# Performance work log

Measured on AMD Instinct MI355X. Metric: run time of the kernel, lower is better.

## Reference

```python
import jax, jax.numpy as jnp
import numpy as np

N, E, F_IN, HID, HEADS, G = 50000, 800000, 128, 128, 4, 512
NEG_SLOPE = 0.2


def setup_inputs() -> dict:
    key = jax.random.key(0)
    ks = jax.random.split(key, 16)
    x = jax.random.normal(ks[0], (N, F_IN), dtype=jnp.float32)
    edge_index = jax.random.randint(ks[1], (2, E), 0, N, dtype=jnp.int32)
    batch = jnp.sort(jax.random.randint(ks[2], (N,), 0, G, dtype=jnp.int32))
    s1 = 1.0 / np.sqrt(F_IN)
    s2 = 1.0 / np.sqrt(HEADS * HID)
    params = {
        "W1": jax.random.uniform(ks[3], (F_IN, HEADS * HID), jnp.float32, -s1, s1),
        "a_src1": jax.random.normal(ks[4], (HEADS, HID), jnp.float32) * s1,
        "a_dst1": jax.random.normal(ks[5], (HEADS, HID), jnp.float32) * s1,
        "b1": jnp.zeros((HEADS * HID,), jnp.float32),
        "W2": jax.random.uniform(ks[6], (HEADS * HID, HID), jnp.float32, -s2, s2),
        "a_src2": jax.random.normal(ks[7], (1, HID), jnp.float32) * s2,
        "a_dst2": jax.random.normal(ks[8], (1, HID), jnp.float32) * s2,
        "b2": jnp.zeros((HID,), jnp.float32),
        "Wl": jax.random.normal(ks[9], (HID, 1), jnp.float32) / np.sqrt(HID),
        "bl": jnp.zeros((1,), jnp.float32),
    }
    return dict(x=x, edge_index=edge_index, batch=batch, **params)


def _gat_conv(x, W, a_src, a_dst, b, src, dst, heads, out_ch):
    n = x.shape[0]
    h = (x @ W).reshape(n, heads, out_ch)                      # [N,H,C]
    asrc = jnp.sum(h * a_src, axis=-1)                          # [N,H]
    adst = jnp.sum(h * a_dst, axis=-1)                          # [N,H]
    logits = jax.nn.leaky_relu(asrc[src] + adst[dst], NEG_SLOPE)  # [E,H]
    m = jax.ops.segment_max(logits, dst, num_segments=n)        # stable softmax per dst
    e = jnp.exp(logits - m[dst])
    denom = jax.ops.segment_sum(e, dst, num_segments=n)
    alpha = e / denom[dst]                                      # [E,H]
    out = jax.ops.segment_sum(alpha[:, :, None] * h[src], dst, num_segments=n)
    return out.reshape(n, heads * out_ch) + b


def reference(x, edge_index, batch, W1, a_src1, a_dst1, b1, W2, a_src2, a_dst2, b2, Wl, bl):
    n = x.shape[0]
    loop = jnp.arange(n, dtype=edge_index.dtype)
    src = jnp.concatenate([edge_index[0], loop])  # add_self_loops=True (PyG default)
    dst = jnp.concatenate([edge_index[1], loop])
    h = _gat_conv(x, W1, a_src1, a_dst1, b1, src, dst, HEADS, HID)
    h = jax.nn.elu(h)
    h = _gat_conv(h, W2, a_src2, a_dst2, b2, src, dst, 1, HID)
    h = jax.nn.elu(h)
    # global_mean_pool
    sums = jax.ops.segment_sum(h, batch, num_segments=G)
    cnts = jax.ops.segment_sum(jnp.ones((n,), h.dtype), batch, num_segments=G)
    pooled = sums / jnp.maximum(cnts, 1.0)[:, None]
    return (pooled @ Wl + bl).squeeze()
```

## Files before the change

### kernel.cpp

```cpp
#include <hip/hip_runtime.h>
#include <math.h>

#define NEG_SLOPE 0.2f

typedef float f4 __attribute__((ext_vector_type(4)));
typedef __attribute__((ext_vector_type(8))) short short8;
typedef __attribute__((ext_vector_type(4))) float f32x4;
typedef unsigned short ushort_t;
typedef unsigned char uchar_t;

__device__ __forceinline__ float bf2f(unsigned short s) {
    unsigned u = ((unsigned)s) << 16;
    float f; __builtin_memcpy(&f, &u, 4); return f;
}
__device__ __forceinline__ unsigned short f2bf(float f) {
    unsigned u; __builtin_memcpy(&u, &f, 4);
    u = (u + 0x7FFFu + ((u >> 16) & 1u)) >> 16;
    return (unsigned short)u;
}
__device__ __forceinline__ void gload16(const void* g, void* l) {
    __builtin_amdgcn_global_load_lds((const __attribute__((address_space(1))) void*)g,
                                     (__attribute__((address_space(3))) void*)l, 16, 0, 0);
}
__device__ __forceinline__ void cvt4(unsigned u, float& a, float& b, float& c, float& d) {
    asm("v_cvt_f32_ubyte0 %0, %1" : "=v"(a) : "v"(u));
    asm("v_cvt_f32_ubyte1 %0, %1" : "=v"(b) : "v"(u));
    asm("v_cvt_f32_ubyte2 %0, %1" : "=v"(c) : "v"(u));
    asm("v_cvt_f32_ubyte3 %0, %1" : "=v"(d) : "v"(u));
}

__global__ void hist_kernel(const int* __restrict__ ei, int E, int Et, int* __restrict__ deg) {
    int e = blockIdx.x * blockDim.x + threadIdx.x;
    if (e >= Et) return;
    int d = (e < E) ? ei[E + e] : (e - E);
    atomicAdd(&deg[d], 1);
}

__global__ __launch_bounds__(1024) void scan_local(const int* __restrict__ deg,
                                                   int* __restrict__ off,
                                                   int* __restrict__ btot, int n) {
    __shared__ int s_w[16];
    int tid = threadIdx.x, lane = tid & 63, wv = tid >> 6;
    int i = blockIdx.x * 1024 + tid;
    int v = (i < n) ? deg[i] : 0;
    int x = v;
    #pragma unroll
    for (int d = 1; d < 64; d <<= 1) {
        int y = __shfl_up(x, d);
        if (lane >= d) x += y;
    }
    if (lane == 63) s_w[wv] = x;
    __syncthreads();
    if (tid < 16) {
        int y = s_w[tid];
        int z = y;
        #pragma unroll
        for (int d = 1; d < 16; d <<= 1) {
            int t2 = __shfl_up(z, d);
            if (tid >= d) z += t2;
        }
        if (tid == 15) btot[blockIdx.x] = z;
        s_w[tid] = z - y;
    }
    __syncthreads();
    if (i < n) off[i] = s_w[wv] + (x - v);
}

__global__ void scan_base(int* __restrict__ btot, int nb) {
    int lane = threadIdx.x;
    int v = (lane < nb) ? btot[lane] : 0;
    int x = v;
    #pragma unroll
    for (int d = 1; d < 64; d <<= 1) {
        int y = __shfl_up(x, d);
        if (lane >= d) x += y;
    }
    int total = __shfl(x, nb - 1);
    if (lane < nb) btot[lane] = x - v;
    if (lane == 0) btot[nb] = total;
}

__global__ void scan_add(const int* __restrict__ btot, int* __restrict__ off,
                         int* __restrict__ cur, const int* __restrict__ batch,
                         int* __restrict__ gcnt, int n, int nb) {
    int i = blockIdx.x * blockDim.x + threadIdx.x;
    if (i < n) {
        int o = off[i] + btot[i >> 10];
        off[i] = o;
        cur[i] = o;
        atomicAdd(&gcnt[batch[i]], 1);
    } else if (i == n) {
        off[n] = btot[nb];
    }
}

__global__ void scatter_kernel(const int* __restrict__ ei, int E, int Et,
                               int* __restrict__ cur, int* __restrict__ csr) {
    int e = blockIdx.x * blockDim.x + threadIdx.x;
    if (e >= Et) return;
    int s, d;
    if (e < E) { s = ei[e]; d = ei[E + e]; }
    else       { s = d = e - E; }
    int p = atomicAdd(&cur[d], 1);
    csr[p] = s;
}

__global__ void cast_all(const float* __restrict__ x, const float* __restrict__ W1,
                         const float* __restrict__ W2, ushort_t* __restrict__ xb,
                         ushort_t* __restrict__ W1t, ushort_t* __restrict__ W2t,
                         int n_x, int pad_x) {
    int i = blockIdx.x * blockDim.x + threadIdx.x;
    if (i < pad_x) {
        xb[i] = f2bf(i < n_x ? x[i] : 0.f);
        return;
    }
    int k = i - pad_x;
    if (k < 128 * 512) {
        int r = k >> 9, c = k & 511;
        W1t[(size_t)c * 128 + r] = f2bf(W1[k]);
        return;
    }
    k -= 128 * 512;
    if (k < 512 * 128) {
        int r = k >> 7, c = k & 127;
        W2t[(size_t)c * 512 + r] = f2bf(W2[k]);
    }
}

template<int H>
__global__ __launch_bounds__(256) void gemm_q128(const ushort_t* __restrict__ A,
                                                 const ushort_t* __restrict__ Bt,
                                                 uchar_t* __restrict__ Cq,
                                                 const float* __restrict__ aw_src,
                                                 const float* __restrict__ aw_dst,
                                                 float* __restrict__ side,
                                                 float* __restrict__ avd,
                                                 int K) {
    const int Nc = H * 128;
    __shared__ __align__(16) ushort_t As[128 * 32];
    __shared__ __align__(16) ushort_t Bs[128 * 32];
    __shared__ float s_red[3][2][128];
    __shared__ float s_rs[128];
    __shared__ __align__(16) uchar_t s_q[128 * 144];
    const int t = threadIdx.x, w = t >> 6, lane = t & 63;
    const int r0 = blockIdx.x * 128, hb = blockIdx.y, c0 = hb * 128;
    const int wr = w & 1, wc = w >> 1;

    const ushort_t* Ag = A + (size_t)(r0 + w * 32 + (lane >> 2)) * K + (lane & 3) * 8;
    const ushort_t* Bg = Bt + (size_t)(c0 + w * 32 + (lane >> 2)) * K + (lane & 3) * 8;
    ushort_t* Al = As + w * 1024;
    ushort_t* Bl = Bs + w * 1024;

    f32x4 acc[4][4] = {};
    for (int k0 = 0; k0 < K; k0 += 32) {
        __syncthreads();
        gload16(Ag + k0, Al);
        gload16(Ag + k0 + (size_t)16 * K, Al + 512);
        gload16(Bg + k0, Bl);
        gload16(Bg + k0 + (size_t)16 * K, Bl + 512);
        __syncthreads();
        short8 af[4], bf[4];
        #pragma unroll
        for (int i = 0; i < 4; i++) {
            af[i] = *(const short8*)(As + (wr * 64 + i * 16 + (lane & 15)) * 32 + (lane >> 4) * 8);
            bf[i] = *(const short8*)(Bs + (wc * 64 + i * 16 + (lane & 15)) * 32 + (lane >> 4) * 8);
        }
        #pragma unroll
        for (int i = 0; i < 4; i++)
            #pragma unroll
            for (int jj = 0; jj < 4; jj++)
                acc[i][jj] = __builtin_amdgcn_mfma_f32_16x16x32_bf16(af[i], bf[jj], acc[i][jj], 0, 0, 0);
    }

    float asc[4], adc[4];
    #pragma unroll
    for (int jj = 0; jj < 4; jj++) {
        int c = c0 + wc * 64 + jj * 16 + (lane & 15);
        asc[jj] = aw_src[c];
        adc[jj] = aw_dst[c];
    }
    #pragma unroll
    for (int i = 0; i < 4; i++) {
        #pragma unroll
        for (int r = 0; r < 4; r++) {
            float m = 0.f, ps = 0.f, pd = 0.f;
            #pragma unroll
            for (int jj = 0; jj < 4; jj++) {
                float v = acc[i][jj][r];
                m = fmaxf(m, fabsf(v));
                ps = fmaf(v, asc[jj], ps);
                pd = fmaf(v, adc[jj], pd);
            }
            #pragma unroll
            for (int d = 1; d < 16; d <<= 1) {
                m = fmaxf(m, __shfl_xor(m, d));
                ps += __shfl_xor(ps, d);
                pd += __shfl_xor(pd, d);
            }
            if ((lane & 15) == 0) {
                int row = wr * 64 + i * 16 + (lane >> 4) * 4 + r;
                s_red[0][wc][row] = m;
                s_red[1][wc][row] = ps;
                s_red[2][wc][row] = pd;
            }
        }
    }
    __syncthreads();
    if (t < 128) {
        float rm = fmaxf(fmaxf(s_red[0][0][t], s_red[0][1][t]), 1e-30f);
        s_rs[t] = 127.f / rm;
        int node = r0 + t;
        side[(size_t)node * (2 * H) + hb]     = s_red[1][0][t] + s_red[1][1][t];
        side[(size_t)node * (2 * H) + H + hb] = rm * (1.f / 127.f);
        avd[(size_t)node * H + hb]            = s_red[2][0][t] + s_red[2][1][t];
    }
    __syncthreads();
    #pragma unroll
    for (int i = 0; i < 4; i++)
        #pragma unroll
        for (int jj = 0; jj < 4; jj++)
            #pragma unroll
            for (int r = 0; r < 4; r++) {
                int row = wr * 64 + i * 16 + (lane >> 4) * 4 + r;
                int col = wc * 64 + jj * 16 + (lane & 15);
                int qi = (int)rintf(acc[i][jj][r] * s_rs[row]) + 128;
                qi = min(255, max(0, qi));
                s_q[row * 144 + col] = (uchar_t)qi;
            }
    __syncthreads();
    #pragma unroll
    for (int p2 = 0; p2 < 4; p2++) {
        int idx = p2 * 256 + t;
        int row = idx >> 3, ch = idx & 7;
        *(uint4*)(Cq + (size_t)(r0 + row) * Nc + c0 + ch * 16) =
            *(const uint4*)(s_q + row * 144 + ch * 16);
    }
}

template<int H, int TOT, bool OUT_BF16>
__global__ __launch_bounds__(256) void agg_q(const int* __restrict__ off,
                                             const int* __restrict__ csr,
                                             const uchar_t* __restrict__ fq,
                                             const float* __restrict__ side,
                                             const float* __restrict__ avd,
                                             const float* __restrict__ bias,
                                             void* __restrict__ outv, int n) {
    constexpr int J = TOT / 64;
    __shared__ float s_e[4][64 * H];
    __shared__ float s_es[4][64 * H];
    int w = threadIdx.x >> 6, lane = threadIdx.x & 63;
    int dst = blockIdx.x * 4 + w;
    if (dst >= n) return;
    const int h_own = (H == 1) ? 0 : (lane >> 4);
    float adv[H];
    if constexpr (H == 4) {
        f4 t4 = *(const f4*)&avd[(size_t)dst * 4];
        #pragma unroll
        for (int h = 0; h < 4; h++) adv[h] = t4[h];
    } else {
        adv[0] = avd[dst];
    }
    int beg = off[dst], end = off[dst + 1];
    float den = 0.f, Ssum = 0.f;
    float acc[J] = {};
    float* ew  = s_e[w];
    float* esw = s_es[w];

    for (int b = beg; b < end; b += 64) {
        int idx = b + lane;
        bool val = idx < end;
        int sv = val ? csr[idx] : 0;
        unsigned myoff = (unsigned)sv * TOT;
        if constexpr (H == 4) {
            const f4* sp = (const f4*)(side + (size_t)sv * 8);
            f4 av = sp[0], sc = sp[1];
            f4 ev, esv;
            #pragma unroll
            for (int h = 0; h < 4; h++) {
                float l = av[h] + adv[h];
                l = fmaxf(l, l * NEG_SLOPE);
                float e = val ? __expf(l) : 0.f;
                ev[h] = e;
                esv[h] = e * sc[h];
            }
            *(f4*)&ew[lane * 4]  = ev;
            *(f4*)&esw[lane * 4] = esv;
        } else {
            float2 sp = *(const float2*)(side + (size_t)sv * 2);
            float l = sp.x + adv[0];
            l = fmaxf(l, l * NEG_SLOPE);
            float e = val ? __expf(l) : 0.f;
            ew[lane]  = e;
            esw[lane] = e * sp.y;
        }
        asm volatile("s_waitcnt lgkmcnt(0)" ::: "memory");
        int cnt = min(64, end - b);
        for (int jb = 0; jb < cnt; jb += 8) {
            uint2 u8v[8];
            unsigned us16[8];
            #pragma unroll
            for (int q = 0; q < 8; q++) {
                unsigned o = (unsigned)__builtin_amdgcn_readlane((int)myoff, jb + q);
                if constexpr (J == 8) {
                    u8v[q] = *(const uint2*)(fq + o + lane * 8);
                } else {
                    us16[q] = *(const ushort_t*)(fq + o + lane * 2);
                }
            }
            #pragma unroll
            for (int q = 0; q < 8; q++) {
                int j = jb + q;
                float e  = ew[j * H + h_own];
                float es = esw[j * H + h_own];
                den += e;
                Ssum += es;
                if constexpr (J == 8) {
                    float b0, b1, b2, b3;
                    cvt4(u8v[q].x, b0, b1, b2, b3);
                    acc[0] = fmaf(es, b0, acc[0]);
                    acc[1] = fmaf(es, b1, acc[1]);
                    acc[2] = fmaf(es, b2, acc[2]);
                    acc[3] = fmaf(es, b3, acc[3]);
                    cvt4(u8v[q].y, b0, b1, b2, b3);
                    acc[4] = fmaf(es, b0, acc[4]);
                    acc[5] = fmaf(es, b1, acc[5]);
                    acc[6] = fmaf(es, b2, acc[6]);
                    acc[7] = fmaf(es, b3, acc[7]);
                } else {
                    float b0, b1;
                    asm("v_cvt_f32_ubyte0 %0, %1" : "=v"(b0) : "v"(us16[q]));
                    asm("v_cvt_f32_ubyte1 %0, %1" : "=v"(b1) : "v"(us16[q]));
                    acc[0] = fmaf(es, b0, acc[0]);
                    acc[1] = fmaf(es, b1, acc[1]);
                }
            }
        }
    }
    float rden = 1.f / den;
    if constexpr (OUT_BF16) {
        unsigned short ov[J];
        #pragma unroll
        for (int u = 0; u < J; u++) {
            float v = (acc[u] - 128.f * Ssum) * rden + bias[lane * J + u];
            v = v > 0.f ? v : expm1f(v);
            ov[u] = f2bf(v);
        }
        *(short8*)((ushort_t*)outv + (size_t)dst * TOT + lane * J) = *(short8*)ov;
    } else {
        float v0 = (acc[0] - 128.f * Ssum) * rden + bias[lane * 2];
        float v1 = (acc[1] - 128.f * Ssum) * rden + bias[lane * 2 + 1];
        v0 = v0 > 0.f ? v0 : expm1f(v0);
        v1 = v1 > 0.f ? v1 : expm1f(v1);
        float2 vv = make_float2(v0, v1);
        *(float2*)((float*)outv + (size_t)dst * TOT + lane * 2) = vv;
    }
}

__global__ __launch_bounds__(256) void pool_kernel(const float* __restrict__ feat,
                                                   const int* __restrict__ batch,
                                                   float* __restrict__ gsum, int n) {
    int t = threadIdx.x;
    int ch = t & 127, half = t >> 7;
    int base = blockIdx.x * 64;
    float acc = 0.f;
    int curg = -1;
    for (int k = half; k < 64; k += 2) {
        int node = base + k;
        if (node >= n) break;
        int g = batch[node];
        if (g != curg) {
            if (curg >= 0) atomicAdd(&gsum[(size_t)curg * 128 + ch], acc);
            acc = 0.f;
            curg = g;
        }
        acc += feat[(size_t)node * 128 + ch];
    }
    if (curg >= 0) atomicAdd(&gsum[(size_t)curg * 128 + ch], acc);
}

__global__ __launch_bounds__(256) void final_kernel(const float* __restrict__ gsum,
                                                    const int* __restrict__ gcnt,
                                                    const float* __restrict__ Wl,
                                                    const float* __restrict__ bl,
                                                    float* __restrict__ out, int g_total) {
    int w = threadIdx.x >> 6, lane = threadIdx.x & 63;
    int g = blockIdx.x * 4 + w;
    if (g >= g_total) return;
    float inv = 1.f / fmaxf((float)gcnt[g], 1.f);
    float p = 0.f;
    #pragma unroll
    for (int j = 0; j < 2; j++) {
        int ch = lane + 64 * j;
        p += gsum[(size_t)g * 128 + ch] * Wl[ch];
    }
    #pragma unroll
    for (int d = 32; d; d >>= 1) p += __shfl_xor(p, d);
    if (lane == 0) out[g] = p * inv + bl[0];
}

extern "C" void kernel_launch(void* const* d_in, const int* in_sizes, int n_in,
                              void* d_out, int out_size, void* d_ws, size_t ws_size,
                              hipStream_t stream) {
    const float* x   = (const float*)d_in[0];
    const int*   ei  = (const int*)d_in[1];
    const int*   bat = (const int*)d_in[2];
    const float* W1  = (const float*)d_in[3];
    const float* as1 = (const float*)d_in[4];
    const float* ad1 = (const float*)d_in[5];
    const float* b1  = (const float*)d_in[6];
    const float* W2  = (const float*)d_in[7];
    const float* as2 = (const float*)d_in[8];
    const float* ad2 = (const float*)d_in[9];
    const float* b2  = (const float*)d_in[10];
    const float* Wl  = (const float*)d_in[11];
    const float* bl  = (const float*)d_in[12];
    float* out = (float*)d_out;

    const int N    = in_sizes[0] / 128;
    const int E    = in_sizes[1] / 2;
    const int Et   = E + N;
    const int G    = 512;
    const int Mpad = (N + 127) & ~127;
    const int nb   = (N + 1023) >> 10;

    char* p = (char*)d_ws;
    auto alloc = [&](size_t bytes) { char* r = p; p += (bytes + 255) & ~(size_t)255; return r; };
    ushort_t* xb    = (ushort_t*)alloc((size_t)Mpad * 128 * 2);
    ushort_t* W1t   = (ushort_t*)alloc((size_t)512 * 128 * 2);
    ushort_t* W2t   = (ushort_t*)alloc((size_t)128 * 512 * 2);
    uchar_t*  h1q   = (uchar_t*)alloc((size_t)Mpad * 512);
    ushort_t* hb    = (ushort_t*)alloc((size_t)Mpad * 512 * 2);
    uchar_t*  h2q   = (uchar_t*)alloc((size_t)Mpad * 128);
    float*    feat2 = (float*)alloc((size_t)N * 128 * 4);
    float*    side1 = (float*)alloc((size_t)Mpad * 8 * 4);
    float*    avd1  = (float*)alloc((size_t)Mpad * 4 * 4);
    float*    side2 = (float*)alloc((size_t)Mpad * 2 * 4);
    float*    avd2  = (float*)alloc((size_t)Mpad * 4);
    float*    gsum  = (float*)alloc((size_t)G * 128 * 4);
    int*      gcnt  = (int*)alloc((size_t)G * 4);
    int*      deg   = (int*)alloc((size_t)N * 4);
    int*      off   = (int*)alloc((size_t)(N + 1) * 4);
    int*      cur   = (int*)alloc((size_t)N * 4);
    int*      btot  = (int*)alloc((size_t)128 * 4);
    int*      csr   = (int*)alloc((size_t)Et * 4);

    hipMemsetAsync(gsum, 0, (size_t)((char*)off - (char*)gsum), stream);
    hipMemsetAsync(hb + (size_t)N * 512, 0, (size_t)(Mpad - N) * 512 * 2, stream);

    hist_kernel<<<(Et + 255) / 256, 256, 0, stream>>>(ei, E, Et, deg);
    scan_local<<<nb, 1024, 0, stream>>>(deg, off, btot, N);
    scan_base<<<1, 64, 0, stream>>>(btot, nb);
    scan_add<<<(N + 256) / 256, 256, 0, stream>>>(btot, off, cur, bat, gcnt, N, nb);
    cast_all<<<((Mpad * 128 + 2 * 65536) + 255) / 256, 256, 0, stream>>>(x, W1, W2, xb, W1t, W2t,
                                                                         N * 128, Mpad * 128);
    scatter_kernel<<<(Et + 255) / 256, 256, 0, stream>>>(ei, E, Et, cur, csr);

    gemm_q128<4><<<dim3(Mpad / 128, 4), 256, 0, stream>>>(xb, W1t, h1q, as1, ad1, side1, avd1, 128);
    agg_q<4, 512, true><<<(N + 3) / 4, 256, 0, stream>>>(off, csr, h1q, side1, avd1, b1, hb, N);

    gemm_q128<1><<<dim3(Mpad / 128, 1), 256, 0, stream>>>(hb, W2t, h2q, as2, ad2, side2, avd2, 512);
    agg_q<1, 128, false><<<(N + 3) / 4, 256, 0, stream>>>(off, csr, h2q, side2, avd2, b2, feat2, N);

    pool_kernel<<<(N + 63) / 64, 256, 0, stream>>>(feat2, bat, gsum, N);
    final_kernel<<<(G + 3) / 4, 256, 0, stream>>>(gsum, gcnt, Wl, bl, out, G);
}
```

Measured before the change: 435.8 us.

## Fuse prep kernels, inline scan base, widen gathers and fuse pooling into aggregation

Merges the degree histogram with the bf16 cast kernel and folds the single-block scan into scan_add, which removes two launches. The aggregation kernel is restructured to use 16-byte gathers: layer 1 processes two edges per wavefront half with double-buffered loads, and layer 2 handles eight edges per pass. Both reduce through cross-lane shuffles. Layer-2 output is no longer written to a feature buffer; it is atomically added straight into per-graph sums, removing pool_kernel and the feat2 round trip. The cost is many more global atomics on gsum (one per node per channel) plus extra shuffle reductions.

```diff
diff --git a/kernel.cpp b/kernel.cpp
--- a/kernel.cpp
+++ b/kernel.cpp
@@ -29,11 +29,31 @@
     asm("v_cvt_f32_ubyte3 %0, %1" : "=v"(d) : "v"(u));
 }
 
-__global__ void hist_kernel(const int* __restrict__ ei, int E, int Et, int* __restrict__ deg) {
-    int e = blockIdx.x * blockDim.x + threadIdx.x;
-    if (e >= Et) return;
-    int d = (e < E) ? ei[E + e] : (e - E);
-    atomicAdd(&deg[d], 1);
+__global__ void prep_kernel(const float* __restrict__ x, const float* __restrict__ W1,
+                            const float* __restrict__ W2, ushort_t* __restrict__ xb,
+                            ushort_t* __restrict__ W1t, ushort_t* __restrict__ W2t,
+                            const int* __restrict__ ei, int* __restrict__ deg,
+                            int n_x, int pad_x, int E, int Et) {
+    int i = blockIdx.x * blockDim.x + threadIdx.x;
+    if (i < Et) {
+        int d = (i < E) ? ei[E + i] : (i - E);
+        atomicAdd(&deg[d], 1);
+    }
+    if (i < pad_x) {
+        xb[i] = f2bf(i < n_x ? x[i] : 0.f);
+        return;
+    }
+    int k = i - pad_x;
+    if (k < 128 * 512) {
+        int r = k >> 9, c = k & 511;
+        W1t[(size_t)c * 128 + r] = f2bf(W1[k]);
+        return;
+    }
+    k -= 128 * 512;
+    if (k < 512 * 128) {
+        int r = k >> 7, c = k & 127;
+        W2t[(size_t)c * 512 + r] = f2bf(W2[k]);
+    }
 }
 
 __global__ __launch_bounds__(1024) void scan_local(const int* __restrict__ deg,
@@ -66,31 +86,35 @@
     if (i < n) off[i] = s_w[wv] + (x - v);
 }
 
-__global__ void scan_base(int* __restrict__ btot, int nb) {
-    int lane = threadIdx.x;
-    int v = (lane < nb) ? btot[lane] : 0;
-    int x = v;
-    #pragma unroll
-    for (int d = 1; d < 64; d <<= 1) {
-        int y = __shfl_up(x, d);
-        if (lane >= d) x += y;
-    }
-    int total = __shfl(x, nb - 1);
-    if (lane < nb) btot[lane] = x - v;
-    if (lane == 0) btot[nb] = total;
-}
-
-__global__ void scan_add(const int* __restrict__ btot, int* __restrict__ off,
-                         int* __restrict__ cur, const int* __restrict__ batch,
-                         int* __restrict__ gcnt, int n, int nb) {
-    int i = blockIdx.x * blockDim.x + threadIdx.x;
+__global__ __launch_bounds__(256) void scan_add(const int* __restrict__ btot,
+                                                int* __restrict__ off,
+                                                int* __restrict__ cur,
+                                                const int* __restrict__ batch,
+                                                int* __restrict__ gcnt, int n, int nb) {
+    __shared__ int s_b[2];
+    int i = blockIdx.x * 256 + threadIdx.x;
+    if (threadIdx.x < 64) {
+        int lane = threadIdx.x;
+        int v = (lane < nb) ? btot[lane] : 0;
+        int x = v;
+        #pragma unroll
+        for (int d = 1; d < 64; d <<= 1) {
+            int y = __shfl_up(x, d);
+            if (lane >= d) x += y;
+        }
+        int c = blockIdx.x >> 2;
+        int base = (c == 0) ? 0 : __shfl(x, c - 1);
+        int total = __shfl(x, nb - 1);
+        if (lane == 0) { s_b[0] = base; s_b[1] = total; }
+    }
+    __syncthreads();
     if (i < n) {
-        int o = off[i] + btot[i >> 10];
+        int o = off[i] + s_b[0];
         off[i] = o;
         cur[i] = o;
         atomicAdd(&gcnt[batch[i]], 1);
     } else if (i == n) {
-        off[n] = btot[nb];
+        off[n] = s_b[1];
     }
 }
 
@@ -103,28 +127,6 @@
     else       { s = d = e - E; }
     int p = atomicAdd(&cur[d], 1);
     csr[p] = s;
-}
-
-__global__ void cast_all(const float* __restrict__ x, const float* __restrict__ W1,
-                         const float* __restrict__ W2, ushort_t* __restrict__ xb,
-                         ushort_t* __restrict__ W1t, ushort_t* __restrict__ W2t,
-                         int n_x, int pad_x) {
-    int i = blockIdx.x * blockDim.x + threadIdx.x;
-    if (i < pad_x) {
-        xb[i] = f2bf(i < n_x ? x[i] : 0.f);
-        return;
-    }
-    int k = i - pad_x;
-    if (k < 128 * 512) {
-        int r = k >> 9, c = k & 511;
-        W1t[(size_t)c * 128 + r] = f2bf(W1[k]);
-        return;
-    }
-    k -= 128 * 512;
-    if (k < 512 * 128) {
-        int r = k >> 7, c = k & 127;
-        W2t[(size_t)c * 512 + r] = f2bf(W2[k]);
-    }
 }
 
 template<int H>
@@ -237,21 +239,21 @@
     }
 }
 
-template<int H, int TOT, bool OUT_BF16>
+template<int H, int TOT, bool OUT_POOL>
 __global__ __launch_bounds__(256) void agg_q(const int* __restrict__ off,
                                              const int* __restrict__ csr,
                                              const uchar_t* __restrict__ fq,
                                              const float* __restrict__ side,
                                              const float* __restrict__ avd,
                                              const float* __restrict__ bias,
-                                             void* __restrict__ outv, int n) {
+                                             ushort_t* __restrict__ outb,
+                                             const int* __restrict__ batch,
+                                             float* __restrict__ gsum, int n) {
     constexpr int J = TOT / 64;
-    __shared__ float s_e[4][64 * H];
-    __shared__ float s_es[4][64 * H];
+    __shared__ __align__(16) float2 s_w[4][64 * H];
     int w = threadIdx.x >> 6, lane = threadIdx.x & 63;
     int dst = blockIdx.x * 4 + w;
     if (dst >= n) return;
-    const int h_own = (H == 1) ? 0 : (lane >> 4);
     float adv[H];
     if constexpr (H == 4) {
         f4 t4 = *(const f4*)&avd[(size_t)dst * 4];
@@ -262,120 +264,162 @@
     }
     int beg = off[dst], end = off[dst + 1];
     float den = 0.f, Ssum = 0.f;
-    float acc[J] = {};
-    float* ew  = s_e[w];
-    float* esw = s_es[w];
+    float acc[16] = {};
+    float2* eww = s_w[w];
+
+    const int half = lane >> 5, sub32 = lane & 31;
+    const int hch  = sub32 >> 3;
+    const int slot = lane >> 3, sub8 = lane & 7;
 
     for (int b = beg; b < end; b += 64) {
         int idx = b + lane;
         bool val = idx < end;
         int sv = val ? csr[idx] : 0;
         unsigned myoff = (unsigned)sv * TOT;
-        if constexpr (H == 4) {
-            const f4* sp = (const f4*)(side + (size_t)sv * 8);
-            f4 av = sp[0], sc = sp[1];
-            f4 ev, esv;
-            #pragma unroll
-            for (int h = 0; h < 4; h++) {
-                float l = av[h] + adv[h];
+        int cnt = min(64, end - b);
+
+        if constexpr (J == 8) {
+            uint4 A[4], B[4];
+            auto issue = [&](int p0, uint4* buf) {
+                #pragma unroll
+                for (int q = 0; q < 4; q++) {
+                    unsigned o = (unsigned)__shfl((int)myoff, (p0 + q) * 2 + half);
+                    buf[q] = *(const uint4*)(fq + o + sub32 * 16);
+                }
+            };
+            int np = (cnt + 1) >> 1;
+            int ng = (np + 3) >> 2;
+            issue(0, A);
+            {
+                const f4* sp = (const f4*)(side + (size_t)sv * 8);
+                f4 av = sp[0], sc = sp[1];
+                f4 ev, esv;
+                #pragma unroll
+                for (int h = 0; h < 4; h++) {
+                    float l = av[h] + adv[h];
+                    l = fmaxf(l, l * NEG_SLOPE);
+                    float e = val ? __expf(l) : 0.f;
+                    ev[h] = e;
+                    esv[h] = e * sc[h];
+                }
+                f4 v01 = {ev[0], esv[0], ev[1], esv[1]};
+                f4 v23 = {ev[2], esv[2], ev[3], esv[3]};
+                *(f4*)&eww[lane * 4]     = v01;
+                *(f4*)&eww[lane * 4 + 2] = v23;
+            }
+            asm volatile("s_waitcnt lgkmcnt(0)" ::: "memory");
+            auto proc = [&](int p0, uint4* buf) {
+                #pragma unroll
+                for (int q = 0; q < 4; q++) {
+                    float2 ees = eww[((p0 + q) * 2 + half) * 4 + hch];
+                    den += ees.x; Ssum += ees.y;
+                    float es = ees.y;
+                    float b0, b1, b2, b3;
+                    cvt4(buf[q].x, b0, b1, b2, b3);
+                    acc[0] = fmaf(es, b0, acc[0]);  acc[1] = fmaf(es, b1, acc[1]);
+                    acc[2] = fmaf(es, b2, acc[2]);  acc[3] = fmaf(es, b3, acc[3]);
+                    cvt4(buf[q].y, b0, b1, b2, b3);
+                    acc[4] = fmaf(es, b0, acc[4]);  acc[5] = fmaf(es, b1, acc[5]);
+                    acc[6] = fmaf(es, b2, acc[6]);  acc[7] = fmaf(es, b3, acc[7]);
+                    cvt4(buf[q].z, b0, b1, b2, b3);
+                    acc[8] = fmaf(es, b0, acc[8]);  acc[9] = fmaf(es, b1, acc[9]);
+                    acc[10] = fmaf(es, b2, acc[10]); acc[11] = fmaf(es, b3, acc[11]);
+                    cvt4(buf[q].w, b0, b1, b2, b3);
+                    acc[12] = fmaf(es, b0, acc[12]); acc[13] = fmaf(es, b1, acc[13]);
+                    acc[14] = fmaf(es, b2, acc[14]); acc[15] = fmaf(es, b3, acc[15]);
+                }
+            };
+            int g = 0;
+            for (;;) {
+                if (g + 1 < ng) issue((g + 1) * 4, B);
+                proc(g * 4, A);
+                if (++g >= ng) break;
+                if (g + 1 < ng) issue((g + 1) * 4, A);
+                proc(g * 4, B);
+                if (++g >= ng) break;
+            }
+        } else {
+            {
+                float2 sp = *(const float2*)(side + (size_t)sv * 2);
+                float l = sp.x + adv[0];
                 l = fmaxf(l, l * NEG_SLOPE);
                 float e = val ? __expf(l) : 0.f;
-                ev[h] = e;
-                esv[h] = e * sc[h];
-            }
-            *(f4*)&ew[lane * 4]  = ev;
-            *(f4*)&esw[lane * 4] = esv;
-        } else {
-            float2 sp = *(const float2*)(side + (size_t)sv * 2);
-            float l = sp.x + adv[0];
-            l = fmaxf(l, l * NEG_SLOPE);
-            float e = val ? __expf(l) : 0.f;
-            ew[lane]  = e;
-            esw[lane] = e * sp.y;
-        }
-        asm volatile("s_waitcnt lgkmcnt(0)" ::: "memory");
-        int cnt = min(64, end - b);
-        for (int jb = 0; jb < cnt; jb += 8) {
-            uint2 u8v[8];
-            unsigned us16[8];
-            #pragma unroll
-            for (int q = 0; q < 8; q++) {
-                unsigned o = (unsigned)__builtin_amdgcn_readlane((int)myoff, jb + q);
-                if constexpr (J == 8) {
-                    u8v[q] = *(const uint2*)(fq + o + lane * 8);
-                } else {
-                    us16[q] = *(const ushort_t*)(fq + o + lane * 2);
+                eww[lane] = make_float2(e, e * sp.y);
+            }
+            asm volatile("s_waitcnt lgkmcnt(0)" ::: "memory");
+            int ng = (cnt + 7) >> 3;
+            uint4 bufs[8];
+            #pragma unroll
+            for (int g = 0; g < 8; g++) {
+                if (g < ng) {
+                    unsigned o = (unsigned)__shfl((int)myoff, g * 8 + slot);
+                    bufs[g] = *(const uint4*)(fq + o + sub8 * 16);
                 }
             }
             #pragma unroll
-            for (int q = 0; q < 8; q++) {
-                int j = jb + q;
-                float e  = ew[j * H + h_own];
-                float es = esw[j * H + h_own];
-                den += e;
-                Ssum += es;
-                if constexpr (J == 8) {
+            for (int g = 0; g < 8; g++) {
+                if (g < ng) {
+                    float2 ees = eww[g * 8 + slot];
+                    den += ees.x; Ssum += ees.y;
+                    float es = ees.y;
                     float b0, b1, b2, b3;
-                    cvt4(u8v[q].x, b0, b1, b2, b3);
-                    acc[0] = fmaf(es, b0, acc[0]);
-                    acc[1] = fmaf(es, b1, acc[1]);
-                    acc[2] = fmaf(es, b2, acc[2]);
-                    acc[3] = fmaf(es, b3, acc[3]);
-                    cvt4(u8v[q].y, b0, b1, b2, b3);
-                    acc[4] = fmaf(es, b0, acc[4]);
-                    acc[5] = fmaf(es, b1, acc[5]);
-                    acc[6] = fmaf(es, b2, acc[6]);
-                    acc[7] = fmaf(es, b3, acc[7]);
-                } else {
-                    float b0, b1;
-                    asm("v_cvt_f32_ubyte0 %0, %1" : "=v"(b0) : "v"(us16[q]));
-                    asm("v_cvt_f32_ubyte1 %0, %1" : "=v"(b1) : "v"(us16[q]));
-                    acc[0] = fmaf(es, b0, acc[0]);
-                    acc[1] = fmaf(es, b1, acc[1]);
+                    cvt4(bufs[g].x, b0, b1, b2, b3);
+                    acc[0] = fmaf(es, b0, acc[0]);  acc[1] = fmaf(es, b1, acc[1]);
+                    acc[2] = fmaf(es, b2, acc[2]);  acc[3] = fmaf(es, b3, acc[3]);
+                    cvt4(bufs[g].y, b0, b1, b2, b3);
+                    acc[4] = fmaf(es, b0, acc[4]);  acc[5] = fmaf(es, b1, acc[5]);
+                    acc[6] = fmaf(es, b2, acc[6]);  acc[7] = fmaf(es, b3, acc[7]);
+                    cvt4(bufs[g].z, b0, b1, b2, b3);
+                    acc[8] = fmaf(es, b0, acc[8]);  acc[9] = fmaf(es, b1, acc[9]);
+                    acc[10] = fmaf(es, b2, acc[10]); acc[11] = fmaf(es, b3, acc[11]);
+                    cvt4(bufs[g].w, b0, b1, b2, b3);
+                    acc[12] = fmaf(es, b0, acc[12]); acc[13] = fmaf(es, b1, acc[13]);
+                    acc[14] = fmaf(es, b2, acc[14]); acc[15] = fmaf(es, b3, acc[15]);
                 }
             }
         }
     }
-    float rden = 1.f / den;
-    if constexpr (OUT_BF16) {
-        unsigned short ov[J];
-        #pragma unroll
-        for (int u = 0; u < J; u++) {
-            float v = (acc[u] - 128.f * Ssum) * rden + bias[lane * J + u];
-            v = v > 0.f ? v : expm1f(v);
-            ov[u] = f2bf(v);
-        }
-        *(short8*)((ushort_t*)outv + (size_t)dst * TOT + lane * J) = *(short8*)ov;
+
+    if constexpr (J == 8) {
+        den += __shfl_xor(den, 32);
+        Ssum += __shfl_xor(Ssum, 32);
+        #pragma unroll
+        for (int u = 0; u < 16; u++) acc[u] += __shfl_xor(acc[u], 32);
+        float rden = 1.f / den;
+        if (half == 0) {
+            unsigned short ov[16];
+            #pragma unroll
+            for (int u = 0; u < 16; u++) {
+                float v = (acc[u] - 128.f * Ssum) * rden + bias[sub32 * 16 + u];
+                v = v > 0.f ? v : expm1f(v);
+                ov[u] = f2bf(v);
+            }
+            ushort_t* op = outb + (size_t)dst * TOT + sub32 * 16;
+            *(short8*)op = *(short8*)ov;
+            *(short8*)(op + 8) = *(short8*)(ov + 8);
+        }
     } else {
-        float v0 = (acc[0] - 128.f * Ssum) * rden + bias[lane * 2];
-        float v1 = (acc[1] - 128.f * Ssum) * rden + bias[lane * 2 + 1];
-        v0 = v0 > 0.f ? v0 : expm1f(v0);
-        v1 = v1 > 0.f ? v1 : expm1f(v1);
-        float2 vv = make_float2(v0, v1);
-        *(float2*)((float*)outv + (size_t)dst * TOT + lane * 2) = vv;
-    }
-}
-
-__global__ __launch_bounds__(256) void pool_kernel(const float* __restrict__ feat,
-                                                   const int* __restrict__ batch,
-                                                   float* __restrict__ gsum, int n) {
-    int t = threadIdx.x;
-    int ch = t & 127, half = t >> 7;
-    int base = blockIdx.x * 64;
-    float acc = 0.f;
-    int curg = -1;
-    for (int k = half; k < 64; k += 2) {
-        int node = base + k;
-        if (node >= n) break;
-        int g = batch[node];
-        if (g != curg) {
-            if (curg >= 0) atomicAdd(&gsum[(size_t)curg * 128 + ch], acc);
-            acc = 0.f;
-            curg = g;
-        }
-        acc += feat[(size_t)node * 128 + ch];
-    }
-    if (curg >= 0) atomicAdd(&gsum[(size_t)curg * 128 + ch], acc);
+        #pragma unroll
+        for (int d = 8; d < 64; d <<= 1) {
+            den += __shfl_xor(den, d);
+            Ssum += __shfl_xor(Ssum, d);
+        }
+        #pragma unroll
+        for (int u = 0; u < 16; u++) {
+            #pragma unroll
+            for (int d = 8; d < 64; d <<= 1) acc[u] += __shfl_xor(acc[u], d);
+        }
+        float rden = 1.f / den;
+        if (lane < 8) {
+            int g = batch[dst];
+            #pragma unroll
+            for (int u = 0; u < 16; u++) {
+                float v = (acc[u] - 128.f * Ssum) * rden + bias[lane * 16 + u];
+                v = v > 0.f ? v : expm1f(v);
+                atomicAdd(&gsum[(size_t)g * 128 + lane * 16 + u], v);
+            }
+        }
+    }
 }
 
 __global__ __launch_bounds__(256) void final_kernel(const float* __restrict__ gsum,
@@ -431,7 +475,6 @@
     uchar_t*  h1q   = (uchar_t*)alloc((size_t)Mpad * 512);
     ushort_t* hb    = (ushort_t*)alloc((size_t)Mpad * 512 * 2);
     uchar_t*  h2q   = (uchar_t*)alloc((size_t)Mpad * 128);
-    float*    feat2 = (float*)alloc((size_t)N * 128 * 4);
     float*    side1 = (float*)alloc((size_t)Mpad * 8 * 4);
     float*    avd1  = (float*)alloc((size_t)Mpad * 4 * 4);
     float*    side2 = (float*)alloc((size_t)Mpad * 2 * 4);
@@ -447,20 +490,20 @@
     hipMemsetAsync(gsum, 0, (size_t)((char*)off - (char*)gsum), stream);
     hipMemsetAsync(hb + (size_t)N * 512, 0, (size_t)(Mpad - N) * 512 * 2, stream);
 
-    hist_kernel<<<(Et + 255) / 256, 256, 0, stream>>>(ei, E, Et, deg);
+    const int prep_n = Mpad * 128 + 2 * 65536;
+    prep_kernel<<<(prep_n + 255) / 256, 256, 0, stream>>>(x, W1, W2, xb, W1t, W2t,
+                                                          ei, deg, N * 128, Mpad * 128, E, Et);
     scan_local<<<nb, 1024, 0, stream>>>(deg, off, btot, N);
-    scan_base<<<1, 64, 0, stream>>>(btot, nb);
     scan_add<<<(N + 256) / 256, 256, 0, stream>>>(btot, off, cur, bat, gcnt, N, nb);
-    cast_all<<<((Mpad * 128 + 2 * 65536) + 255) / 256, 256, 0, stream>>>(x, W1, W2, xb, W1t, W2t,
-                                                                         N * 128, Mpad * 128);
     scatter_kernel<<<(Et + 255) / 256, 256, 0, stream>>>(ei, E, Et, cur, csr);
 
     gemm_q128<4><<<dim3(Mpad / 128, 4), 256, 0, stream>>>(xb, W1t, h1q, as1, ad1, side1, avd1, 128);
-    agg_q<4, 512, true><<<(N + 3) / 4, 256, 0, stream>>>(off, csr, h1q, side1, avd1, b1, hb, N);
+    agg_q<4, 512, false><<<(N + 3) / 4, 256, 0, stream>>>(off, csr, h1q, side1, avd1, b1, hb,
+                                                          nullptr, nullptr, N);
 
     gemm_q128<1><<<dim3(Mpad / 128, 1), 256, 0, stream>>>(hb, W2t, h2q, as2, ad2, side2, avd2, 512);
-    agg_q<1, 128, false><<<(N + 3) / 4, 256, 0, stream>>>(off, csr, h2q, side2, avd2, b2, feat2, N);
-
-    pool_kernel<<<(N + 63) / 64, 256, 0, stream>>>(feat2, bat, gsum, N);
+    agg_q<1, 128, true><<<(N + 3) / 4, 256, 0, stream>>>(off, csr, h2q, side2, avd2, b2, nullptr,
+                                                         bat, gsum, N);
+
     final_kernel<<<(G + 3) / 4, 256, 0, stream>>>(gsum, gcnt, Wl, bl, out, G);
 }
```

After: 827.2 us. 1.9x slower.
